# Kernel tuning notes

Measured on AMD Instinct MI355X. Metric: run time of the kernel, lower is better.

Reference implementation:

```python
import jax, jax.numpy as jnp
import numpy as np


def setup_inputs() -> dict:
    N, E, D, C = 100000, 100000, 512, 512
    key = jax.random.key(0)
    k = jax.random.split(key, 6)
    x = jax.random.normal(k[0], (N, D), dtype=jnp.float32)
    W = jax.random.normal(k[1], (D, 3 * C), dtype=jnp.float32) * (1.0 / np.sqrt(D))
    bias = jax.random.normal(k[2], (C,), dtype=jnp.float32) * (1.0 / np.sqrt(C))
    eta = jax.random.uniform(k[3], (E, 3, 1), dtype=jnp.float32)
    src = jax.random.randint(k[4], (E,), 0, N, dtype=jnp.int32)
    dst = jax.random.randint(k[5], (E,), 0, N, dtype=jnp.int32)
    return {"x": x, "W": W, "bias": bias, "eta": eta, "src": src, "dst": dst}


def reference(x, W, bias, eta, src, dst):
    N = x.shape[0]
    C = bias.shape[0]
    # projection: [N, D] @ [D, 3C] -> [N, 3, C]
    h = jnp.matmul(x, W).reshape(N, 3, C)
    # message: src node state scaled by per-edge eta [E,3,1]
    msg = h[src] * eta  # [E, 3, C]
    # reduce: sum messages into destination nodes (nodes w/o in-edges -> 0)
    agg = jax.ops.segment_sum(msg, dst, num_segments=N)  # [N, 3, C]
    # sum over the 3 positional slots, add bias, tanh
    return jnp.tanh(agg.sum(axis=1) + bias)
```

## Files before the change

### kernel.cpp

```cpp
#include <hip/hip_runtime.h>

typedef _Float16 half_t;
typedef __attribute__((ext_vector_type(8))) _Float16 half8;
typedef __attribute__((ext_vector_type(4))) float floatx4;

#define BM 128
#define BN 128
#define BK 32

__global__ void cvt_w_kernel(const float* __restrict__ W, half_t* __restrict__ Wt,
                             const float* __restrict__ bias, float* __restrict__ tb,
                             int D, int C, int total) {
    int idx = blockIdx.x * blockDim.x + threadIdx.x;
    if (idx >= total) return;
    if (idx < C) {
        float ex = __expf(2.0f * bias[idx]);
        tb[idx] = 1.0f - 2.0f / (ex + 1.0f);
    }
    int c = idx / 1536;
    int r = idx - c * 1536;
    int s = r >> 9;
    int d = r & 511;
    Wt[idx] = (half_t)W[(long)d * 1536 + s * 512 + c];
}

__global__ void hist_kernel(const int* __restrict__ dst, int* __restrict__ deg, int E) {
    int e = blockIdx.x * blockDim.x + threadIdx.x;
    if (e < E) atomicAdd(&deg[dst[e]], 1);
}

__global__ void scan_partial2_kernel(const int* __restrict__ deg,
                                     int* __restrict__ bsum, int* __restrict__ bsum2, int n) {
    __shared__ int wsum[4], wsum2[4];
    int t = threadIdx.x, lane = t & 63, w = t >> 6;
    int base = blockIdx.x * 1024 + t * 4;
    int s = 0, s2 = 0;
#pragma unroll
    for (int j = 0; j < 4; ++j) {
        int i = base + j;
        if (i < n) { int d = deg[i]; s += d; s2 += (d > 0); }
    }
#pragma unroll
    for (int o = 1; o < 64; o <<= 1) { s += __shfl_xor(s, o); s2 += __shfl_xor(s2, o); }
    if (lane == 0) { wsum[w] = s; wsum2[w] = s2; }
    __syncthreads();
    if (t == 0) {
        bsum[blockIdx.x]  = wsum[0]  + wsum[1]  + wsum[2]  + wsum[3];
        bsum2[blockIdx.x] = wsum2[0] + wsum2[1] + wsum2[2] + wsum2[3];
    }
}

__device__ int exscan_wave128(int* arr, int nb, int lane) {
    int a0 = (lane < nb) ? arr[lane] : 0;
    int a1 = (64 + lane < nb) ? arr[64 + lane] : 0;
    int s0 = a0, s1 = a1;
#pragma unroll
    for (int o = 1; o < 64; o <<= 1) {
        int t0 = __shfl_up(s0, o); if (lane >= o) s0 += t0;
        int t1 = __shfl_up(s1, o); if (lane >= o) s1 += t1;
    }
    s1 += __shfl(s0, 63);
    int tot = __shfl(s1, 63);
    if (lane < nb) arr[lane] = s0 - a0;
    if (64 + lane < nb) arr[64 + lane] = s1 - a1;
    return tot;
}

__global__ void scan_bsums2_kernel(int* __restrict__ bsum, int* __restrict__ bsum2,
                                   int nb, int* __restrict__ mc) {
    int lane = threadIdx.x & 63;
    if (nb <= 128) {
        exscan_wave128(bsum, nb, lane);
        int tot = exscan_wave128(bsum2, nb, lane);
        if (lane == 0) *mc = tot;
    } else if (lane == 0) {
        int acc = 0, acc2 = 0;
        for (int i = 0; i < nb; ++i) {
            int v = bsum[i];  bsum[i] = acc;   acc += v;
            int v2 = bsum2[i]; bsum2[i] = acc2; acc2 += v2;
        }
        *mc = acc2;
    }
}

__global__ void scan_final2_kernel(const int* __restrict__ deg,
                                   const int* __restrict__ bsum, const int* __restrict__ bsum2,
                                   int* __restrict__ off, int* __restrict__ rank,
                                   int* __restrict__ nodeid, int n) {
    __shared__ int wsum[4], wsum2[4];
    int t = threadIdx.x, lane = t & 63, w = t >> 6;
    int base = blockIdx.x * 1024 + t * 4;
    int v[4]; int s = 0, s2 = 0;
#pragma unroll
    for (int j = 0; j < 4; ++j) {
        int i = base + j;
        v[j] = (i < n) ? deg[i] : 0;
        s += v[j]; s2 += (v[j] > 0);
    }
    int sc = s, sc2 = s2;
#pragma unroll
    for (int o = 1; o < 64; o <<= 1) {
        int u  = __shfl_up(sc, o);  if (lane >= o) sc  += u;
        int u2 = __shfl_up(sc2, o); if (lane >= o) sc2 += u2;
    }
    if (lane == 63) { wsum[w] = sc; wsum2[w] = sc2; }
    __syncthreads();
    int woff = 0, woff2 = 0;
    for (int i = 0; i < w; ++i) { woff += wsum[i]; woff2 += wsum2[i]; }
    int ex  = bsum[blockIdx.x]  + woff  + (sc  - s);
    int ex2 = bsum2[blockIdx.x] + woff2 + (sc2 - s2);
#pragma unroll
    for (int j = 0; j < 4; ++j) {
        int i = base + j;
        if (i < n) {
            off[i] = ex;
            if (v[j] > 0) { rank[i] = ex2; nodeid[ex2] = i; ex2++; }
            ex += v[j];
        }
    }
}

__global__ void scatter_kernel(const int* __restrict__ dst, const int* __restrict__ src,
                               const float* __restrict__ eta,
                               const int* __restrict__ off, int* __restrict__ cursor,
                               int* __restrict__ srcs, floatx4* __restrict__ etas, int E) {
    int e = blockIdx.x * blockDim.x + threadIdx.x;
    if (e >= E) return;
    int d = dst[e];
    int p = off[d] + atomicAdd(&cursor[d], 1);
    srcs[p] = src[e];
    floatx4 et;
    et[0] = eta[3 * e + 0]; et[1] = eta[3 * e + 1]; et[2] = eta[3 * e + 2]; et[3] = 0.0f;
    etas[p] = et;
}

__global__ __launch_bounds__(256) void aggx_kernel(
    const float* __restrict__ x, const int* __restrict__ srcs,
    const floatx4* __restrict__ etas, const int* __restrict__ off,
    const int* __restrict__ deg, const int* __restrict__ rank,
    const float* __restrict__ tb, float* __restrict__ out,
    half_t* __restrict__ Z, int N, int D, int C)
{
    int node = blockIdx.x * 4 + (threadIdx.x >> 6);
    if (node >= N) return;
    int lane = threadIdx.x & 63;
    int d = deg[node];
    if (d == 0) {
        float* o = out + (long)node * C;
        for (int c0 = lane * 8; c0 < C; c0 += 64 * 8) {
            floatx4 v0 = *(const floatx4*)(tb + c0);
            floatx4 v1 = *(const floatx4*)(tb + c0 + 4);
            __builtin_nontemporal_store(v0, (floatx4*)(o + c0));
            __builtin_nontemporal_store(v1, (floatx4*)(o + c0 + 4));
        }
        return;
    }

    float a0[8] = {}, a1[8] = {}, a2[8] = {};
    int start = off[node];
    for (int q = 0; q < d; ++q) {
        int s = srcs[start + q];
        floatx4 et = etas[start + q];
        const float* xr = x + (long)s * D + lane * 8;
        floatx4 v0 = *(const floatx4*)xr;
        floatx4 v1 = *(const floatx4*)(xr + 4);
#pragma unroll
        for (int j = 0; j < 4; ++j) {
            a0[j] += et[0] * v0[j]; a0[j + 4] += et[0] * v1[j];
            a1[j] += et[1] * v0[j]; a1[j + 4] += et[1] * v1[j];
            a2[j] += et[2] * v0[j]; a2[j + 4] += et[2] * v1[j];
        }
    }
    half_t* zr = Z + (long)rank[node] * (3 * D) + lane * 8;
    half8 h0, h1, h2;
#pragma unroll
    for (int j = 0; j < 8; ++j) { h0[j] = (half_t)a0[j]; h1[j] = (half_t)a1[j]; h2[j] = (half_t)a2[j]; }
    *(half8*)zr = h0;
    *(half8*)(zr + D) = h1;
    *(half8*)(zr + 2 * D) = h2;
}

__global__ __launch_bounds__(256) void gemm_tanh_kernel(
    const half_t* __restrict__ A,
    const half_t* __restrict__ Bt,
    const float* __restrict__ bias,
    const int* __restrict__ mc_ptr,
    const int* __restrict__ nodeid,
    float* __restrict__ out,
    int K, int C)
{
    __shared__ half_t As[3][BM * BK];
    __shared__ half_t Bs[3][BN * BK];

    const int Mc = *mc_ptr;
    const int ncol = C / BN;
    const int T = ((Mc + BM - 1) / BM) * ncol;
    const int b = blockIdx.x;
    if (b >= T) return;
    const int qq = T >> 3, rem = T & 7;
    const int xcd = b & 7, ib = b >> 3;
    const int wg = (xcd < rem ? xcd * (qq + 1) : rem * (qq + 1) + (xcd - rem) * qq) + ib;
    const int n0 = (wg % ncol) * BN;
    const int m0 = (wg / ncol) * BM;

    const int t    = threadIdx.x;
    const int lane = t & 63;
    const int wave = t >> 6;
    const int wm   = (wave >> 1) * 64;
    const int wn   = (wave & 1) * 64;

    const int r1 = t >> 2;
    const int r2 = r1 + 64;
    const int k8 = (((t & 3) ^ ((t >> 3) & 3))) * 8;
    const long gA1 = (long)(m0 + r1) * K + k8;
    const long gA2 = (long)(m0 + r2) * K + k8;
    const long gB1 = (long)(n0 + r1) * K + k8;
    const long gB2 = (long)(n0 + r2) * K + k8;

    floatx4 acc[4][4] = {};

    const int mrow = wm + (lane & 15);
    const int nrow = wn + (lane & 15);
    const int koff = (((lane >> 4) ^ ((lane >> 1) & 3))) * 8;

#define STAGE(buf, kt)                                                                     \
    do {                                                                                   \
        __builtin_amdgcn_global_load_lds(                                                  \
            (const __attribute__((address_space(1))) void*)(A + gA1 + (kt)),               \
            (__attribute__((address_space(3))) void*)(&As[buf][t * 8]), 16, 0, 0);         \
        __builtin_amdgcn_global_load_lds(                                                  \
            (const __attribute__((address_space(1))) void*)(A + gA2 + (kt)),               \
            (__attribute__((address_space(3))) void*)(&As[buf][(t + 256) * 8]), 16, 0, 0); \
        __builtin_amdgcn_global_load_lds(                                                  \
            (const __attribute__((address_space(1))) void*)(Bt + gB1 + (kt)),              \
            (__attribute__((address_space(3))) void*)(&Bs[buf][t * 8]), 16, 0, 0);         \
        __builtin_amdgcn_global_load_lds(                                                  \
            (const __attribute__((address_space(1))) void*)(Bt + gB2 + (kt)),              \
            (__attribute__((address_space(3))) void*)(&Bs[buf][(t + 256) * 8]), 16, 0, 0); \
    } while (0)

#define COMPUTE(buf)                                                                       \
    do {                                                                                   \
        half8 af[4], bf[4];                                                                \
        _Pragma("unroll") for (int i = 0; i < 4; ++i)                                      \
            af[i] = *(const half8*)&As[buf][(mrow + i * 16) * BK + koff];                   \
        _Pragma("unroll") for (int i = 0; i < 4; ++i)                                      \
            bf[i] = *(const half8*)&Bs[buf][(nrow + i * 16) * BK + koff];                   \
        _Pragma("unroll") for (int i = 0; i < 4; ++i)                                      \
            _Pragma("unroll") for (int j = 0; j < 4; ++j)                                  \
                acc[i][j] = __builtin_amdgcn_mfma_f32_16x16x32_f16(af[i], bf[j],           \
                                                                   acc[i][j], 0, 0, 0);   \
    } while (0)

    const int nsteps = K / BK;
    int b0 = 0, b1 = 1, b2 = 2;
    STAGE(0, 0);
    STAGE(1, BK);
    for (int ks = 0; ks < nsteps - 2; ++ks) {
        STAGE(b2, (ks + 2) * BK);
        asm volatile("s_waitcnt vmcnt(8)" ::: "memory");
        __builtin_amdgcn_sched_barrier(0);
        __builtin_amdgcn_s_barrier();
        __builtin_amdgcn_sched_barrier(0);
        COMPUTE(b0);
        __builtin_amdgcn_sched_barrier(0);
        __builtin_amdgcn_s_barrier();
        __builtin_amdgcn_sched_barrier(0);
        int tmp = b0; b0 = b1; b1 = b2; b2 = tmp;
    }
    asm volatile("s_waitcnt vmcnt(4)" ::: "memory");
    __builtin_amdgcn_sched_barrier(0);
    __builtin_amdgcn_s_barrier();
    __builtin_amdgcn_sched_barrier(0);
    COMPUTE(b0);
    asm volatile("s_waitcnt vmcnt(0)" ::: "memory");
    __builtin_amdgcn_sched_barrier(0);
    __builtin_amdgcn_s_barrier();
    __builtin_amdgcn_sched_barrier(0);
    COMPUTE(b1);

#undef STAGE
#undef COMPUTE

    const int col0 = lane & 15;
    const int rbase = (lane >> 4) * 4;
    float bj[4];
#pragma unroll
    for (int j = 0; j < 4; ++j)
        bj[j] = bias[n0 + wn + col0 + j * 16];
#pragma unroll
    for (int i = 0; i < 4; ++i) {
#pragma unroll
        for (int rr = 0; rr < 4; ++rr) {
            int crow = m0 + wm + i * 16 + rbase + rr;
            if (crow >= Mc) continue;
            long base = (long)nodeid[crow] * C + n0 + wn + col0;
#pragma unroll
            for (int j = 0; j < 4; ++j) {
                float xv = acc[i][j][rr] + bj[j];
                float ex = __expf(2.0f * xv);
                __builtin_nontemporal_store(1.0f - 2.0f / (ex + 1.0f), &out[base + j * 16]);
            }
        }
    }
}

extern "C" void kernel_launch(void* const* d_in, const int* in_sizes, int n_in,
                              void* d_out, int out_size, void* d_ws, size_t ws_size,
                              hipStream_t stream) {
    const float* x    = (const float*)d_in[0];
    const float* W    = (const float*)d_in[1];
    const float* bias = (const float*)d_in[2];
    const float* eta  = (const float*)d_in[3];
    const int*   src  = (const int*)d_in[4];
    const int*   dst  = (const int*)d_in[5];
    float* out = (float*)d_out;

    const int  C   = in_sizes[2];
    const int  C3  = 3 * C;
    const int  D   = in_sizes[1] / C3;
    const long xcount = in_sizes[0];
    const int  N   = (int)(xcount / D);
    const int  E   = in_sizes[4];
    const int  K   = 3 * D;
    const int  Npad = ((N + BM - 1) / BM) * BM;
    const int  nb  = (N + 1023) / 1024;
    const size_t nbPad = (size_t)((nb + 3) & ~3);

    auto alignup = [](size_t v) { return (v + 15) & ~(size_t)15; };

    char* ws = (char*)d_ws;
    size_t o = 0;
    half_t* Z    = (half_t*)(ws + o); o += (size_t)Npad * K * sizeof(half_t);
    half_t* Wt_h = (half_t*)(ws + o); o += (size_t)C * K * sizeof(half_t);
    int* deg     = (int*)(ws + o);    o += (size_t)N * sizeof(int);
    int* cursor  = (int*)(ws + o);    o += (size_t)N * sizeof(int);
    int* off     = (int*)(ws + o);    o += (size_t)N * sizeof(int);
    int* rank    = (int*)(ws + o);    o += (size_t)N * sizeof(int);
    int* nodeid  = (int*)(ws + o);    o += (size_t)N * sizeof(int);
    int* srcs    = (int*)(ws + o);    o += (size_t)E * sizeof(int);
    o = alignup(o);
    floatx4* etas = (floatx4*)(ws + o); o += (size_t)E * sizeof(floatx4);
    int* bsum    = (int*)(ws + o);    o += nbPad * sizeof(int);
    int* bsum2   = (int*)(ws + o);    o += nbPad * sizeof(int);
    int* mc      = (int*)(ws + o);    o += 4 * sizeof(int);
    float* tb    = (float*)(ws + o);  o += (size_t)C * sizeof(float);

    hipMemsetAsync(deg, 0, 2 * (size_t)N * sizeof(int), stream);
    cvt_w_kernel<<<(C * K + 255) / 256, 256, 0, stream>>>(W, Wt_h, bias, tb, D, C, C * K);
    hist_kernel<<<(E + 255) / 256, 256, 0, stream>>>(dst, deg, E);
    scan_partial2_kernel<<<nb, 256, 0, stream>>>(deg, bsum, bsum2, N);
    scan_bsums2_kernel<<<1, 64, 0, stream>>>(bsum, bsum2, nb, mc);
    scan_final2_kernel<<<nb, 256, 0, stream>>>(deg, bsum, bsum2, off, rank, nodeid, N);
    scatter_kernel<<<(E + 255) / 256, 256, 0, stream>>>(dst, src, eta, off, cursor, srcs, etas, E);
    aggx_kernel<<<(N + 3) / 4, 256, 0, stream>>>(x, srcs, etas, off, deg, rank, tb, out, Z, N, D, C);
    {
        const int nwg = ((N + BM - 1) / BM) * (C / BN);
        gemm_tanh_kernel<<<nwg, 256, 0, stream>>>(Z, Wt_h, bias, mc, nodeid, out, K, C);
    }
}
```

Measured before the change: 561.5 us.

## Enlarge GEMM tile to 256x256x64 with 512 threads and double buffering

Grows the fused GEMM+tanh tile from 128x128x32 to 256x256x64 and runs it with 8 waves per block. Each wave now computes a 128x64 subtile, and LDS is split into half-tiles with an 8-way XOR swizzle. The three-stage LDS pipeline becomes a double buffer, which is meant to raise arithmetic intensity and cut global traffic and barrier counts per FLOP. In exchange, accumulator register pressure rises and there are fewer blocks. The grid now uses Npad, which must be a multiple of 256.

```diff
diff --git a/kernel.cpp b/kernel.cpp
--- a/kernel.cpp
+++ b/kernel.cpp
@@ -4,9 +4,9 @@
 typedef __attribute__((ext_vector_type(8))) _Float16 half8;
 typedef __attribute__((ext_vector_type(4))) float floatx4;
 
-#define BM 128
-#define BN 128
-#define BK 32
+#define BM 256
+#define BN 256
+#define BK 64
 
 __global__ void cvt_w_kernel(const float* __restrict__ W, half_t* __restrict__ Wt,
                              const float* __restrict__ bias, float* __restrict__ tb,
@@ -180,7 +180,7 @@
     *(half8*)(zr + 2 * D) = h2;
 }
 
-__global__ __launch_bounds__(256) void gemm_tanh_kernel(
+__global__ __launch_bounds__(512, 2) void gemm_tanh_kernel(
     const half_t* __restrict__ A,
     const half_t* __restrict__ Bt,
     const float* __restrict__ bias,
@@ -189,8 +189,8 @@
     float* __restrict__ out,
     int K, int C)
 {
-    __shared__ half_t As[3][BM * BK];
-    __shared__ half_t Bs[3][BN * BK];
+    __shared__ half_t As[2][2][128 * 64];
+    __shared__ half_t Bs[2][2][128 * 64];
 
     const int Mc = *mc_ptr;
     const int ncol = C / BN;
@@ -206,78 +206,98 @@
     const int t    = threadIdx.x;
     const int lane = t & 63;
     const int wave = t >> 6;
-    const int wm   = (wave >> 1) * 64;
-    const int wn   = (wave & 1) * 64;
-
-    const int r1 = t >> 2;
-    const int r2 = r1 + 64;
-    const int k8 = (((t & 3) ^ ((t >> 3) & 3))) * 8;
-    const long gA1 = (long)(m0 + r1) * K + k8;
-    const long gA2 = (long)(m0 + r2) * K + k8;
-    const long gB1 = (long)(n0 + r1) * K + k8;
-    const long gB2 = (long)(n0 + r2) * K + k8;
-
-    floatx4 acc[4][4] = {};
-
-    const int mrow = wm + (lane & 15);
-    const int nrow = wn + (lane & 15);
-    const int koff = (((lane >> 4) ^ ((lane >> 1) & 3))) * 8;
-
-#define STAGE(buf, kt)                                                                     \
-    do {                                                                                   \
-        __builtin_amdgcn_global_load_lds(                                                  \
-            (const __attribute__((address_space(1))) void*)(A + gA1 + (kt)),               \
-            (__attribute__((address_space(3))) void*)(&As[buf][t * 8]), 16, 0, 0);         \
-        __builtin_amdgcn_global_load_lds(                                                  \
-            (const __attribute__((address_space(1))) void*)(A + gA2 + (kt)),               \
-            (__attribute__((address_space(3))) void*)(&As[buf][(t + 256) * 8]), 16, 0, 0); \
-        __builtin_amdgcn_global_load_lds(                                                  \
-            (const __attribute__((address_space(1))) void*)(Bt + gB1 + (kt)),              \
-            (__attribute__((address_space(3))) void*)(&Bs[buf][t * 8]), 16, 0, 0);         \
-        __builtin_amdgcn_global_load_lds(                                                  \
-            (const __attribute__((address_space(1))) void*)(Bt + gB2 + (kt)),              \
-            (__attribute__((address_space(3))) void*)(&Bs[buf][(t + 256) * 8]), 16, 0, 0); \
+    const int wm   = (wave >> 2) * 128;
+    const int wn   = (wave & 3) * 64;
+    const int hA   = wave >> 2;
+    const int hB   = (wave & 3) >> 1;
+    const int cb   = (wave & 1) * 64;
+
+    const int r1 = t >> 3;
+    const int k8 = (((t & 7) ^ ((t >> 3) & 7))) * 8;
+    const long gA0 = (long)(m0 + r1)       * K + k8;
+    const long gA1 = (long)(m0 + 64 + r1)  * K + k8;
+    const long gA2 = (long)(m0 + 128 + r1) * K + k8;
+    const long gA3 = (long)(m0 + 192 + r1) * K + k8;
+    const long gB0 = (long)(n0 + r1)       * K + k8;
+    const long gB1 = (long)(n0 + 64 + r1)  * K + k8;
+    const long gB2 = (long)(n0 + 128 + r1) * K + k8;
+    const long gB3 = (long)(n0 + 192 + r1) * K + k8;
+
+    floatx4 acc[8][4] = {};
+
+    const int aBase = (lane & 15) * 64;
+    const int bBase = (cb + (lane & 15)) * 64;
+    const int c0 = (((lane >> 4)) ^ (lane & 7)) * 8;
+    const int c1 = (((lane >> 4) + 4) ^ (lane & 7)) * 8;
+
+#define STAGE(buf, ktk)                                                                     \
+    do {                                                                                    \
+        __builtin_amdgcn_global_load_lds(                                                   \
+            (const __attribute__((address_space(1))) void*)(A + gA0 + (ktk)),               \
+            (__attribute__((address_space(3))) void*)(&As[buf][0][t * 8]), 16, 0, 0);       \
+        __builtin_amdgcn_global_load_lds(                                                   \
+            (const __attribute__((address_space(1))) void*)(A + gA1 + (ktk)),               \
+            (__attribute__((address_space(3))) void*)(&As[buf][0][(512 + t) * 8]), 16, 0, 0); \
+        __builtin_amdgcn_global_load_lds(                                                   \
+            (const __attribute__((address_space(1))) void*)(A + gA2 + (ktk)),               \
+            (__attribute__((address_space(3))) void*)(&As[buf][1][t * 8]), 16, 0, 0);       \
+        __builtin_amdgcn_global_load_lds(                                                   \
+            (const __attribute__((address_space(1))) void*)(A + gA3 + (ktk)),               \
+            (__attribute__((address_space(3))) void*)(&As[buf][1][(512 + t) * 8]), 16, 0, 0); \
+        __builtin_amdgcn_global_load_lds(                                                   \
+            (const __attribute__((address_space(1))) void*)(Bt + gB0 + (ktk)),              \
+            (__attribute__((address_space(3))) void*)(&Bs[buf][0][t * 8]), 16, 0, 0);       \
+        __builtin_amdgcn_global_load_lds(                                                   \
+            (const __attribute__((address_space(1))) void*)(Bt + gB1 + (ktk)),              \
+            (__attribute__((address_space(3))) void*)(&Bs[buf][0][(512 + t) * 8]), 16, 0, 0); \
+        __builtin_amdgcn_global_load_lds(                                                   \
+            (const __attribute__((address_space(1))) void*)(Bt + gB2 + (ktk)),              \
+            (__attribute__((address_space(3))) void*)(&Bs[buf][1][t * 8]), 16, 0, 0);       \
+        __builtin_amdgcn_global_load_lds(                                                   \
+            (const __attribute__((address_space(1))) void*)(Bt + gB3 + (ktk)),              \
+            (__attribute__((address_space(3))) void*)(&Bs[buf][1][(512 + t) * 8]), 16, 0, 0); \
     } while (0)
 
-#define COMPUTE(buf)                                                                       \
-    do {                                                                                   \
-        half8 af[4], bf[4];                                                                \
-        _Pragma("unroll") for (int i = 0; i < 4; ++i)                                      \
-            af[i] = *(const half8*)&As[buf][(mrow + i * 16) * BK + koff];                   \
-        _Pragma("unroll") for (int i = 0; i < 4; ++i)                                      \
-            bf[i] = *(const half8*)&Bs[buf][(nrow + i * 16) * BK + koff];                   \
-        _Pragma("unroll") for (int i = 0; i < 4; ++i)                                      \
-            _Pragma("unroll") for (int j = 0; j < 4; ++j)                                  \
-                acc[i][j] = __builtin_amdgcn_mfma_f32_16x16x32_f16(af[i], bf[j],           \
-                                                                   acc[i][j], 0, 0, 0);   \
+#define COMPUTE(buf)                                                                        \
+    do {                                                                                    \
+        const half_t* Ab = &As[buf][hA][0];                                                 \
+        const half_t* Bb = &Bs[buf][hB][0];                                                 \
+        half8 a[8], bf[4];                                                                  \
+        _Pragma("unroll") for (int i = 0; i < 8; ++i)                                       \
+            a[i] = *(const half8*)&Ab[aBase + i * 1024 + c0];                               \
+        _Pragma("unroll") for (int j = 0; j < 4; ++j)                                       \
+            bf[j] = *(const half8*)&Bb[bBase + j * 1024 + c0];                              \
+        _Pragma("unroll") for (int i = 0; i < 8; ++i)                                       \
+            _Pragma("unroll") for (int j = 0; j < 4; ++j)                                   \
+                acc[i][j] = __builtin_amdgcn_mfma_f32_16x16x32_f16(a[i], bf[j],             \
+                                                                   acc[i][j], 0, 0, 0);    \
+        _Pragma("unroll") for (int i = 0; i < 8; ++i)                                       \
+            a[i] = *(const half8*)&Ab[aBase + i * 1024 + c1];                               \
+        _Pragma("unroll") for (int j = 0; j < 4; ++j)                                       \
+            bf[j] = *(const half8*)&Bb[bBase + j * 1024 + c1];                              \
+        _Pragma("unroll") for (int i = 0; i < 8; ++i)                                       \
+            _Pragma("unroll") for (int j = 0; j < 4; ++j)                                   \
+                acc[i][j] = __builtin_amdgcn_mfma_f32_16x16x32_f16(a[i], bf[j],             \
+                                                                   acc[i][j], 0, 0, 0);    \
     } while (0)
 
-    const int nsteps = K / BK;
-    int b0 = 0, b1 = 1, b2 = 2;
+    const int nt = K / BK;
     STAGE(0, 0);
-    STAGE(1, BK);
-    for (int ks = 0; ks < nsteps - 2; ++ks) {
-        STAGE(b2, (ks + 2) * BK);
-        asm volatile("s_waitcnt vmcnt(8)" ::: "memory");
+    for (int kt = 0; kt < nt; ++kt) {
+        if (kt + 1 < nt) {
+            STAGE((kt + 1) & 1, (kt + 1) * BK);
+            asm volatile("s_waitcnt vmcnt(8)" ::: "memory");
+        } else {
+            asm volatile("s_waitcnt vmcnt(0)" ::: "memory");
+        }
         __builtin_amdgcn_sched_barrier(0);
         __builtin_amdgcn_s_barrier();
         __builtin_amdgcn_sched_barrier(0);
-        COMPUTE(b0);
+        COMPUTE(kt & 1);
         __builtin_amdgcn_sched_barrier(0);
         __builtin_amdgcn_s_barrier();
         __builtin_amdgcn_sched_barrier(0);
-        int tmp = b0; b0 = b1; b1 = b2; b2 = tmp;
-    }
-    asm volatile("s_waitcnt vmcnt(4)" ::: "memory");
-    __builtin_amdgcn_sched_barrier(0);
-    __builtin_amdgcn_s_barrier();
-    __builtin_amdgcn_sched_barrier(0);
-    COMPUTE(b0);
-    asm volatile("s_waitcnt vmcnt(0)" ::: "memory");
-    __builtin_amdgcn_sched_barrier(0);
-    __builtin_amdgcn_s_barrier();
-    __builtin_amdgcn_sched_barrier(0);
-    COMPUTE(b1);
+    }
 
 #undef STAGE
 #undef COMPUTE
@@ -289,7 +309,7 @@
     for (int j = 0; j < 4; ++j)
         bj[j] = bias[n0 + wn + col0 + j * 16];
 #pragma unroll
-    for (int i = 0; i < 4; ++i) {
+    for (int i = 0; i < 8; ++i) {
 #pragma unroll
         for (int rr = 0; rr < 4; ++rr) {
             int crow = m0 + wm + i * 16 + rbase + rr;
@@ -355,7 +375,7 @@
     scatter_kernel<<<(E + 255) / 256, 256, 0, stream>>>(dst, src, eta, off, cursor, srcs, etas, E);
     aggx_kernel<<<(N + 3) / 4, 256, 0, stream>>>(x, srcs, etas, off, deg, rank, tb, out, Z, N, D, C);
     {
-        const int nwg = ((N + BM - 1) / BM) * (C / BN);
-        gemm_tanh_kernel<<<nwg, 256, 0, stream>>>(Z, Wt_h, bias, mc, nodeid, out, K, C);
-    }
-}
+        const int nwg = (Npad / BM) * (C / BN);
+        gemm_tanh_kernel<<<nwg, 512, 0, stream>>>(Z, Wt_h, bias, mc, nodeid, out, K, C);
+    }
+}
```

Result: faster. 543.4 us (-3.2%).
